# Optimization experiments

Hardware: AMD Instinct MI355X
Metric: run time of the kernel (lower is better)

## Reference

```python
import jax, jax.numpy as jnp
import numpy as np

T = 8           # hardcoded frame count in forward
MAX_D = 3       # hardcoded displacement radius -> 7x7 = 49-entry cost volume
PATCH = 2 * MAX_D + 1
EPS = 1e-12     # F.normalize eps


def _l2norm_c(x):
    # x: [B, C, H, W]; L2-normalize over channel dim (torch F.normalize dim=1)
    n = jnp.sqrt(jnp.sum(x * x, axis=1, keepdims=True))
    return x / jnp.maximum(n, EPS)


def setup_inputs() -> dict:
    key = jax.random.key(0)
    ks = jax.random.split(key, 6)
    B, N, C = 2, 8192, 512
    nh = 8
    d = C // nh
    return {
        "x": jax.random.normal(ks[0], (B, N, C), jnp.float32),
        "w_qk": jax.random.normal(ks[1], (2 * C, C), jnp.float32) * 0.02,
        "w_corr": jax.random.normal(ks[2], (d, PATCH * PATCH), jnp.float32) * 0.02,
        "b_corr": jax.random.normal(ks[3], (d,), jnp.float32) * 0.02,
        "w_proj": jax.random.normal(ks[4], (C, C), jnp.float32) * 0.02,
        "b_proj": jax.random.normal(ks[5], (C,), jnp.float32) * 0.02,
    }


def reference(x, w_qk, w_corr, b_corr, w_proj, b_proj):
    B, N, C = x.shape
    nh = 8
    d = C // nh
    H = int(round((N // T) ** 0.5))
    W = H

    # qk projection (no bias): [B, N, 2C] -> [2, B, nh, N, d]
    qk = jnp.einsum('bnc,ec->bne', x, w_qk).reshape(B, N, 2, nh, d)
    q = jnp.transpose(qk[:, :, 0], (0, 2, 1, 3))  # [B, nh, N, d]
    k = jnp.transpose(qk[:, :, 1], (0, 2, 1, 3))

    # 'b n (t h w) d -> (b n) t d h w'
    def to_vid(a):
        a = a.reshape(B, nh, T, H, W, d)
        return jnp.transpose(a, (0, 1, 2, 5, 3, 4)).reshape(B * nh, T, d, H, W)

    q = to_vid(q)
    k = to_vid(k)

    # k_postfix: shift time forward, repeat last frame
    k_post = jnp.concatenate([k[:, 1:], k[:, -1:]], axis=1)

    BT = B * nh * T
    qf = _l2norm_c(q.reshape(BT, d, H, W))
    kf = _l2norm_c(k_post.reshape(BT, d, H, W))

    # local cost volume: corr[b, u*7+v, y, x] = sum_c qf[b,c,y,x] * kf[b,c,y+u-3,x+v-3]
    kp = jnp.pad(kf, ((0, 0), (0, 0), (MAX_D, MAX_D), (MAX_D, MAX_D)))
    corr = jnp.stack(
        [jnp.sum(qf * kp[:, :, u:u + H, v:v + W], axis=1)
         for u in range(PATCH) for v in range(PATCH)],
        axis=1,
    )  # [BT, 49, H, W]

    # 'b u v h w -> b (h w) (u v)'
    corr = jnp.transpose(corr, (0, 2, 3, 1)).reshape(BT, H * W, PATCH * PATCH)

    # proj_corr: 49 -> head_dim
    mf = jnp.einsum('bpk,dk->bpd', corr, w_corr) + b_corr  # [BT, HW, d]

    # '(b n t) (h w) d -> b (t h w) (n d)'
    mf = mf.reshape(B, nh, T, H, W, d)
    mf = jnp.transpose(mf, (0, 2, 3, 4, 1, 5)).reshape(B, N, C)

    # final projection
    return jnp.einsum('bnc,oc->bno', mf, w_proj) + b_proj
```

## Files before the change

kernel.cpp:

```cpp
#include <hip/hip_runtime.h>

typedef unsigned int u32;
typedef unsigned short u16;
typedef __fp16 h2 __attribute__((ext_vector_type(2)));
typedef __fp16 f16x8 __attribute__((ext_vector_type(8)));
typedef float f32x4 __attribute__((ext_vector_type(4)));

#define DEVFN static __device__ __forceinline__

DEVFN u32 pkh(float a, float b) {
  return __builtin_bit_cast(u32, __builtin_amdgcn_cvt_pkrtz(a, b));
}
DEVFN u16 f2h(float f) { __fp16 h = (__fp16)f; return __builtin_bit_cast(u16, h); }

#if __has_builtin(__builtin_amdgcn_fdot2)
DEVFN float dot2u(u32 a, u32 b, float c) {
  return __builtin_amdgcn_fdot2(__builtin_bit_cast(h2, a),
                                __builtin_bit_cast(h2, b), c, false);
}
#else
DEVFN float dot2u(u32 a, u32 b, float c) {
  h2 x = __builtin_bit_cast(h2, a), y = __builtin_bit_cast(h2, b);
  return c + (float)x[0] * (float)y[0] + (float)x[1] * (float)y[1];
}
#endif

DEVFN uint4 cvt8h(const float* p) {
  f32x4 v0 = *(const f32x4*)p;
  f32x4 v1 = *(const f32x4*)(p + 4);
  uint4 o;
  o.x = pkh(v0.x, v0.y); o.y = pkh(v0.z, v0.w);
  o.z = pkh(v1.x, v1.y); o.w = pkh(v1.z, v1.w);
  return o;
}

DEVFN void gld16(const u16* g, u16* l) {
  __builtin_amdgcn_global_load_lds(
      (const __attribute__((address_space(1))) u32*)g,
      (__attribute__((address_space(3))) u32*)l, 16, 0, 0);
}

__global__ __launch_bounds__(256) void cvt3(
    const float* __restrict__ x, const float* __restrict__ wqk,
    u16* __restrict__ xb, u16* __restrict__ wqb) {
  const size_t e = ((size_t)blockIdx.x * 256 + threadIdx.x) * 8;
  const float* s;
  u16* d;
  if (e < 8388608) { s = x + e; d = xb + e; }
  else { s = wqk + (e - 8388608); d = wqb + (e - 8388608); }
  *(uint4*)d = cvt8h(s);
}

__global__ __launch_bounds__(512) void w2prep(
    const float* __restrict__ wp, const float* __restrict__ wc,
    const float* __restrict__ bc, const float* __restrict__ bp,
    u16* __restrict__ W2, float* __restrict__ cvec) {
  __shared__ float wcl[64 * 49];
  __shared__ float wpl[512];
  const int o = blockIdx.x, tid = threadIdx.x;
  for (int i = tid; i < 64 * 49; i += 512) wcl[i] = wc[i];
  wpl[tid] = wp[o * 512 + tid];
  __syncthreads();
  const int hh = tid >> 6, r = tid & 63, du = r >> 3, dv = r & 7;
  float s = 0.f;
  if (du < 7 && dv < 7) {
#pragma unroll
    for (int c = 0; c < 64; ++c) s += wpl[hh * 64 + c] * wcl[c * 49 + du * 7 + dv];
  }
  W2[o * 512 + tid] = f2h(s);
  if (tid < 64) {
    float p = 0.f;
#pragma unroll
    for (int g = 0; g < 8; ++g) p += wpl[g * 64 + tid];
    p *= bc[tid];
    p += __shfl_xor(p, 1); p += __shfl_xor(p, 2); p += __shfl_xor(p, 4);
    p += __shfl_xor(p, 8); p += __shfl_xor(p, 16); p += __shfl_xor(p, 32);
    if (tid == 0) cvec[o] = p + bp[o];
  }
}

template <int MODE, int TN>
__global__ __launch_bounds__(256) void gemm(
    const u16* __restrict__ A, const u16* __restrict__ B,
    const float* __restrict__ bias, void* __restrict__ Out_,
    int Nn, int K) {
  __shared__ u16 As[128 * 32];
  __shared__ u16 Bs[128 * 32];
  const int tid = threadIdx.x;
  const int lane = tid & 63;
  const int w = tid >> 6;
  const int wm = w >> 1, wn = w & 1;
  const int nwg = (int)gridDim.x;
  const int wg = ((int)blockIdx.x & 7) * (nwg >> 3) + ((int)blockIdx.x >> 3);
  const int tm = wg / TN, tn = wg % TN;

  const int sr = w * 32 + (lane >> 2);
  const int sc = (lane & 3) << 3;
  u16* lA = As + w * 1024;
  u16* lB = Bs + w * 1024;
  const u16* gA = A + (size_t)(tm * 128 + sr) * K + sc;
  const u16* gB = B + (size_t)(tn * 128 + sr) * K + sc;

  const u16* rA = As + (wm * 64 + (lane & 15)) * 32 + ((lane >> 4) << 3);
  const u16* rB = Bs + (wn * 64 + (lane & 15)) * 32 + ((lane >> 4) << 3);

  f32x4 acc[4][4] = {};

  const int KT = K >> 5;
  for (int kt = 0; kt < KT; ++kt) {
    __syncthreads();
    gld16(gA + kt * 32, lA);
    gld16(gA + kt * 32 + (size_t)16 * K, lA + 512);
    gld16(gB + kt * 32, lB);
    gld16(gB + kt * 32 + (size_t)16 * K, lB + 512);
    __syncthreads();
    f16x8 af[4], bf[4];
#pragma unroll
    for (int i = 0; i < 4; ++i) af[i] = *(const f16x8*)(rA + i * 512);
#pragma unroll
    for (int i = 0; i < 4; ++i) bf[i] = *(const f16x8*)(rB + i * 512);
#pragma unroll
    for (int mi = 0; mi < 4; ++mi)
#pragma unroll
      for (int ni = 0; ni < 4; ++ni)
        acc[mi][ni] = __builtin_amdgcn_mfma_f32_16x16x32_f16(af[mi], bf[ni],
                                                             acc[mi][ni], 0, 0, 0);
  }

  const int rowBase = tm * 128 + wm * 64 + ((lane >> 4) << 2);
  const int colBase = tn * 128 + wn * 64 + (lane & 15);

  if (MODE == 1) {
    float* Out = (float*)Out_;
    float bv[4];
#pragma unroll
    for (int ni = 0; ni < 4; ++ni) bv[ni] = bias[colBase + ni * 16];
#pragma unroll
    for (int mi = 0; mi < 4; ++mi)
#pragma unroll
      for (int r = 0; r < 4; ++r) {
        size_t ro = (size_t)(rowBase + mi * 16 + r) * Nn;
#pragma unroll
        for (int ni = 0; ni < 4; ++ni)
          Out[ro + colBase + ni * 16] = acc[mi][ni][r] + bv[ni];
      }
  } else {
    u16* Out = (u16*)Out_;
    const int sel = colBase >> 9;
    const int hh = (colBase >> 6) & 7;
    const int ddb = lane & 15;
#pragma unroll
    for (int mi = 0; mi < 4; ++mi)
#pragma unroll
      for (int r = 0; r < 4; ++r) {
        float s = acc[mi][0][r] * acc[mi][0][r] + acc[mi][1][r] * acc[mi][1][r] +
                  acc[mi][2][r] * acc[mi][2][r] + acc[mi][3][r] * acc[mi][3][r];
        s += __shfl_xor(s, 1);
        s += __shfl_xor(s, 2);
        s += __shfl_xor(s, 4);
        s += __shfl_xor(s, 8);
        float inv = 1.0f / fmaxf(sqrtf(s), 1e-12f);
        const int m = rowBase + mi * 16 + r;
        const int bb = m >> 13, tt = (m >> 10) & 7, pix = m & 1023;
        const int fr = ((sel * 2 + bb) * 8 + tt) * 8 + hh;
        size_t base = (((size_t)fr) << 16) + (size_t)pix * 64 + ddb;
#pragma unroll
        for (int ni = 0; ni < 4; ++ni)
          Out[base + ni * 16] = f2h(acc[mi][ni][r] * inv);
      }
  }
}

__global__ __launch_bounds__(256) void dots(
    const u16* __restrict__ qf, u16* __restrict__ corr) {
  __shared__ __align__(16) u16 kst[448 * 64];
  const int tid = threadIdx.x;
  const int bid = ((int)blockIdx.x & 7) * 64 + ((int)blockIdx.x >> 3);
  const int fr = bid >> 2, grp = bid & 3;
  const int h = fr & 7, t = (fr >> 3) & 7, b = fr >> 6;
  const int t1 = (t < 7) ? t + 1 : 7;
  const int y0 = grp * 8;

  const u16* kbase = qf + (((size_t)(((2 + b) * 8 + t1) * 8 + h)) << 16);
  {
    const int ppx = tid >> 3;
    const int slot = tid & 7;
#pragma unroll
    for (int pass = 0; pass < 14; ++pass) {
      int gy = y0 - 3 + pass;
      uint4 v = make_uint4(0, 0, 0, 0);
      if ((unsigned)gy < 32u)
        v = *(const uint4*)(kbase + (size_t)(gy * 32 + ppx) * 64 + slot * 8);
      int pl = pass * 32 + ppx;
      *(uint4*)((char*)kst + pl * 128 + ((slot * 16) ^ ((pl & 7) << 4))) = v;
    }
  }

  const int px = grp * 256 + tid;
  const int x = tid & 31, yloc = tid >> 5;
  const u16* qp = qf + (((size_t)fr) << 16) + (size_t)px * 64;
  u32 qw[32];
#pragma unroll
  for (int j = 0; j < 8; ++j) {
    uint4 v = *(const uint4*)(qp + j * 8);
    qw[j * 4 + 0] = v.x; qw[j * 4 + 1] = v.y;
    qw[j * 4 + 2] = v.z; qw[j * 4 + 3] = v.w;
  }
  __syncthreads();

  u16* mp = corr + (size_t)((b * 8 + t) * 1024 + px) * 512 + h * 64;
  for (int du = 0; du < 7; ++du) {
    const int rlbase = (yloc + du) * 32;
    float f[7];
#pragma unroll
    for (int dv = 0; dv < 7; ++dv) {
      int xx = x + dv - 3;
      int xc = xx < 0 ? 0 : (xx > 31 ? 31 : xx);
      int pl = rlbase + xc;
      const char* kr = (const char*)kst + pl * 128;
      const int swz = (pl & 7) << 4;
      float s0 = 0.f, s1 = 0.f, s2 = 0.f, s3 = 0.f;
#pragma unroll
      for (int j = 0; j < 8; ++j) {
        uint4 v = *(const uint4*)(kr + ((j * 16) ^ swz));
        s0 = dot2u(qw[j * 4 + 0], v.x, s0);
        s1 = dot2u(qw[j * 4 + 1], v.y, s1);
        s2 = dot2u(qw[j * 4 + 2], v.z, s2);
        s3 = dot2u(qw[j * 4 + 3], v.w, s3);
      }
      float s = (s0 + s1) + (s2 + s3);
      f[dv] = ((unsigned)xx < 32u) ? s : 0.f;
    }
    uint4 o;
    o.x = pkh(f[0], f[1]); o.y = pkh(f[2], f[3]);
    o.z = pkh(f[4], f[5]); o.w = pkh(f[6], 0.f);
    *(uint4*)(mp + du * 8) = o;
  }
  *(uint4*)(mp + 56) = make_uint4(0, 0, 0, 0);
}

extern "C" void kernel_launch(void* const* d_in, const int* in_sizes, int n_in,
                              void* d_out, int out_size, void* d_ws, size_t ws_size,
                              hipStream_t stream) {
  const float* x      = (const float*)d_in[0];
  const float* w_qk   = (const float*)d_in[1];
  const float* w_corr = (const float*)d_in[2];
  const float* b_corr = (const float*)d_in[3];
  const float* w_proj = (const float*)d_in[4];
  const float* b_proj = (const float*)d_in[5];
  float* out = (float*)d_out;

  u16* xb   = (u16*)d_ws;
  u16* corr = xb;
  u16* qf   = (u16*)d_ws + (size_t)16384 * 512;
  u16* W2   = qf;
  float* cvec = (float*)(qf + (size_t)512 * 512);
  u16* wqb  = (u16*)d_out;

  cvt3<<<dim3(4352), dim3(256), 0, stream>>>(x, w_qk, xb, wqb);
  gemm<0, 8><<<dim3(1024), dim3(256), 0, stream>>>(xb, wqb, nullptr, qf,
                                                   1024, 512);
  dots<<<dim3(512), dim3(256), 0, stream>>>(qf, corr);
  w2prep<<<dim3(512), dim3(512), 0, stream>>>(w_proj, w_corr, b_corr, b_proj,
                                              W2, cvec);
  gemm<1, 4><<<dim3(512), dim3(256), 0, stream>>>(corr, W2, cvec, out,
                                                  512, 512);
}
```

Measured before the change: 91.37 us.

## Fuse fp32-to-fp16 conversion into QK GEMM loads and double-buffer LDS

Drops the separate conversion kernel that turned x and w_qk into fp16 in workspace. The QK GEMM now reads fp32 directly from global memory and packs it to fp16 in registers before storing to shared memory. Both GEMMs also gain a double-buffered LDS pipeline that prefetches the next K tile while the MFMAs run on the current one, leaving one barrier per iteration. This removes a kernel launch and a full fp16 write-then-read of the activations, but the QK GEMM reads twice the bytes per tile and uses more registers and shared memory.

```diff
diff --git a/kernel.cpp b/kernel.cpp
--- a/kernel.cpp
+++ b/kernel.cpp
@@ -25,12 +25,10 @@
 }
 #endif
 
-DEVFN uint4 cvt8h(const float* p) {
-  f32x4 v0 = *(const f32x4*)p;
-  f32x4 v1 = *(const f32x4*)(p + 4);
+DEVFN uint4 pk8(f32x4 lo, f32x4 hi) {
   uint4 o;
-  o.x = pkh(v0.x, v0.y); o.y = pkh(v0.z, v0.w);
-  o.z = pkh(v1.x, v1.y); o.w = pkh(v1.z, v1.w);
+  o.x = pkh(lo.x, lo.y); o.y = pkh(lo.z, lo.w);
+  o.z = pkh(hi.x, hi.y); o.w = pkh(hi.z, hi.w);
   return o;
 }
 
@@ -38,17 +36,6 @@
   __builtin_amdgcn_global_load_lds(
       (const __attribute__((address_space(1))) u32*)g,
       (__attribute__((address_space(3))) u32*)l, 16, 0, 0);
-}
-
-__global__ __launch_bounds__(256) void cvt3(
-    const float* __restrict__ x, const float* __restrict__ wqk,
-    u16* __restrict__ xb, u16* __restrict__ wqb) {
-  const size_t e = ((size_t)blockIdx.x * 256 + threadIdx.x) * 8;
-  const float* s;
-  u16* d;
-  if (e < 8388608) { s = x + e; d = xb + e; }
-  else { s = wqk + (e - 8388608); d = wqb + (e - 8388608); }
-  *(uint4*)d = cvt8h(s);
 }
 
 __global__ __launch_bounds__(512) void w2prep(
@@ -79,13 +66,13 @@
   }
 }
 
-template <int MODE, int TN>
+template <int MODE, int AF32, int BF32, int TN>
 __global__ __launch_bounds__(256) void gemm(
-    const u16* __restrict__ A, const u16* __restrict__ B,
+    const void* __restrict__ A_, const void* __restrict__ B_,
     const float* __restrict__ bias, void* __restrict__ Out_,
     int Nn, int K) {
-  __shared__ u16 As[128 * 32];
-  __shared__ u16 Bs[128 * 32];
+  __shared__ u16 As[2][128 * 32];
+  __shared__ u16 Bs[2][128 * 32];
   const int tid = threadIdx.x;
   const int lane = tid & 63;
   const int w = tid >> 6;
@@ -94,37 +81,103 @@
   const int wg = ((int)blockIdx.x & 7) * (nwg >> 3) + ((int)blockIdx.x >> 3);
   const int tm = wg / TN, tn = wg % TN;
 
+  const float* Af = (const float*)A_;
+  const float* Bf = (const float*)B_;
+  const u16* Ah = (const u16*)A_;
+  const u16* Bh = (const u16*)B_;
+
   const int sr = w * 32 + (lane >> 2);
   const int sc = (lane & 3) << 3;
-  u16* lA = As + w * 1024;
-  u16* lB = Bs + w * 1024;
-  const u16* gA = A + (size_t)(tm * 128 + sr) * K + sc;
-  const u16* gB = B + (size_t)(tn * 128 + sr) * K + sc;
-
-  const u16* rA = As + (wm * 64 + (lane & 15)) * 32 + ((lane >> 4) << 3);
-  const u16* rB = Bs + (wn * 64 + (lane & 15)) * 32 + ((lane >> 4) << 3);
+  const u16* gA = Ah + (size_t)(tm * 128 + sr) * K + sc;
+  const u16* gB = Bh + (size_t)(tn * 128 + sr) * K + sc;
+  u16* lA = &As[0][0] + w * 1024;
+  u16* lB = &Bs[0][0] + w * 1024;
+
+  const int rr = tid >> 2;
+  const int rc = (tid & 3) << 3;
+  const size_t offA0 = (size_t)(tm * 128 + rr) * K + rc;
+  const size_t offB0 = (size_t)(tn * 128 + rr) * K + rc;
+  u16* sA0 = &As[0][0] + rr * 32 + rc;
+  u16* sB0 = &Bs[0][0] + rr * 32 + rc;
+
+  const u16* rA = &As[0][0] + (wm * 64 + (lane & 15)) * 32 + ((lane >> 4) << 3);
+  const u16* rB = &Bs[0][0] + (wn * 64 + (lane & 15)) * 32 + ((lane >> 4) << 3);
 
   f32x4 acc[4][4] = {};
-
   const int KT = K >> 5;
+
+  if (AF32) {
+    f32x4 p0 = *(const f32x4*)(Af + offA0);
+    f32x4 p1 = *(const f32x4*)(Af + offA0 + 4);
+    f32x4 p2 = *(const f32x4*)(Af + offA0 + (size_t)64 * K);
+    f32x4 p3 = *(const f32x4*)(Af + offA0 + (size_t)64 * K + 4);
+    *(uint4*)sA0 = pk8(p0, p1);
+    *(uint4*)(sA0 + 2048) = pk8(p2, p3);
+  } else {
+    gld16(gA, lA);
+    gld16(gA + (size_t)16 * K, lA + 512);
+  }
+  if (BF32) {
+    f32x4 p0 = *(const f32x4*)(Bf + offB0);
+    f32x4 p1 = *(const f32x4*)(Bf + offB0 + 4);
+    f32x4 p2 = *(const f32x4*)(Bf + offB0 + (size_t)64 * K);
+    f32x4 p3 = *(const f32x4*)(Bf + offB0 + (size_t)64 * K + 4);
+    *(uint4*)sB0 = pk8(p0, p1);
+    *(uint4*)(sB0 + 2048) = pk8(p2, p3);
+  } else {
+    gld16(gB, lB);
+    gld16(gB + (size_t)16 * K, lB + 512);
+  }
+  __syncthreads();
+
   for (int kt = 0; kt < KT; ++kt) {
-    __syncthreads();
-    gld16(gA + kt * 32, lA);
-    gld16(gA + kt * 32 + (size_t)16 * K, lA + 512);
-    gld16(gB + kt * 32, lB);
-    gld16(gB + kt * 32 + (size_t)16 * K, lB + 512);
-    __syncthreads();
+    const int cur = kt & 1, nxt = cur ^ 1;
+    const bool more = (kt + 1) < KT;
+    f32x4 a0, a1, a2, a3, b0, b1, b2, b3;
+    if (more) {
+      const int off = (kt + 1) * 32;
+      if (AF32) {
+        a0 = *(const f32x4*)(Af + offA0 + off);
+        a1 = *(const f32x4*)(Af + offA0 + off + 4);
+        a2 = *(const f32x4*)(Af + offA0 + off + (size_t)64 * K);
+        a3 = *(const f32x4*)(Af + offA0 + off + (size_t)64 * K + 4);
+      } else {
+        gld16(gA + off, lA + nxt * 4096);
+        gld16(gA + off + (size_t)16 * K, lA + nxt * 4096 + 512);
+      }
+      if (BF32) {
+        b0 = *(const f32x4*)(Bf + offB0 + off);
+        b1 = *(const f32x4*)(Bf + offB0 + off + 4);
+        b2 = *(const f32x4*)(Bf + offB0 + off + (size_t)64 * K);
+        b3 = *(const f32x4*)(Bf + offB0 + off + (size_t)64 * K + 4);
+      } else {
+        gld16(gB + off, lB + nxt * 4096);
+        gld16(gB + off + (size_t)16 * K, lB + nxt * 4096 + 512);
+      }
+    }
+
     f16x8 af[4], bf[4];
 #pragma unroll
-    for (int i = 0; i < 4; ++i) af[i] = *(const f16x8*)(rA + i * 512);
-#pragma unroll
-    for (int i = 0; i < 4; ++i) bf[i] = *(const f16x8*)(rB + i * 512);
+    for (int i = 0; i < 4; ++i) af[i] = *(const f16x8*)(rA + cur * 4096 + i * 512);
+#pragma unroll
+    for (int i = 0; i < 4; ++i) bf[i] = *(const f16x8*)(rB + cur * 4096 + i * 512);
 #pragma unroll
     for (int mi = 0; mi < 4; ++mi)
 #pragma unroll
       for (int ni = 0; ni < 4; ++ni)
         acc[mi][ni] = __builtin_amdgcn_mfma_f32_16x16x32_f16(af[mi], bf[ni],
                                                              acc[mi][ni], 0, 0, 0);
+    if (more) {
+      if (AF32) {
+        *(uint4*)(sA0 + nxt * 4096) = pk8(a0, a1);
+        *(uint4*)(sA0 + nxt * 4096 + 2048) = pk8(a2, a3);
+      }
+      if (BF32) {
+        *(uint4*)(sB0 + nxt * 4096) = pk8(b0, b1);
+        *(uint4*)(sB0 + nxt * 4096 + 2048) = pk8(b2, b3);
+      }
+    }
+    __syncthreads();
   }
 
   const int rowBase = tm * 128 + wm * 64 + ((lane >> 4) << 2);
@@ -250,19 +303,16 @@
   const float* b_proj = (const float*)d_in[5];
   float* out = (float*)d_out;
 
-  u16* xb   = (u16*)d_ws;
-  u16* corr = xb;
-  u16* qf   = (u16*)d_ws + (size_t)16384 * 512;
+  u16* corr = (u16*)d_ws;
+  u16* qf   = corr + (size_t)16384 * 512;
   u16* W2   = qf;
   float* cvec = (float*)(qf + (size_t)512 * 512);
-  u16* wqb  = (u16*)d_out;
-
-  cvt3<<<dim3(4352), dim3(256), 0, stream>>>(x, w_qk, xb, wqb);
-  gemm<0, 8><<<dim3(1024), dim3(256), 0, stream>>>(xb, wqb, nullptr, qf,
-                                                   1024, 512);
+
+  gemm<0, 1, 1, 8><<<dim3(1024), dim3(256), 0, stream>>>(
+      x, w_qk, nullptr, qf, 1024, 512);
   dots<<<dim3(512), dim3(256), 0, stream>>>(qf, corr);
   w2prep<<<dim3(512), dim3(512), 0, stream>>>(w_proj, w_corr, b_corr, b_proj,
                                               W2, cvec);
-  gemm<1, 4><<<dim3(512), dim3(256), 0, stream>>>(corr, W2, cvec, out,
-                                                  512, 512);
-}
+  gemm<1, 0, 0, 4><<<dim3(512), dim3(256), 0, stream>>>(
+      corr, W2, cvec, out, 512, 512);
+}
```

After: 83.73 us. 8.4% less time.

## Fuse fp32->fp16 conversion into GEMM loads, double-buffer LDS, merge weight prep

Applied to the files above, without the earlier changes.

Removes the standalone conversion kernel. The first GEMM now reads fp32 x and w_qk directly and packs them to fp16 into LDS, which avoids writing and re-reading the fp16 copies. The GEMM switches from global_load_lds to register-staged loads with double-buffered LDS, prefetching two tiles ahead so loads overlap MFMA work. The weight-combination prep is folded into the cost-volume kernel as extra blocks, cutting one launch. The trade-offs are more register pressure and twice the fp32 global traffic per tile in the first GEMM.

```diff
diff --git a/kernel.cpp b/kernel.cpp
--- a/kernel.cpp
+++ b/kernel.cpp
@@ -25,67 +25,20 @@
 }
 #endif
 
-DEVFN uint4 cvt8h(const float* p) {
-  f32x4 v0 = *(const f32x4*)p;
-  f32x4 v1 = *(const f32x4*)(p + 4);
+DEVFN uint4 pk8(f32x4 lo, f32x4 hi) {
   uint4 o;
-  o.x = pkh(v0.x, v0.y); o.y = pkh(v0.z, v0.w);
-  o.z = pkh(v1.x, v1.y); o.w = pkh(v1.z, v1.w);
+  o.x = pkh(lo.x, lo.y); o.y = pkh(lo.z, lo.w);
+  o.z = pkh(hi.x, hi.y); o.w = pkh(hi.z, hi.w);
   return o;
 }
 
-DEVFN void gld16(const u16* g, u16* l) {
-  __builtin_amdgcn_global_load_lds(
-      (const __attribute__((address_space(1))) u32*)g,
-      (__attribute__((address_space(3))) u32*)l, 16, 0, 0);
-}
-
-__global__ __launch_bounds__(256) void cvt3(
-    const float* __restrict__ x, const float* __restrict__ wqk,
-    u16* __restrict__ xb, u16* __restrict__ wqb) {
-  const size_t e = ((size_t)blockIdx.x * 256 + threadIdx.x) * 8;
-  const float* s;
-  u16* d;
-  if (e < 8388608) { s = x + e; d = xb + e; }
-  else { s = wqk + (e - 8388608); d = wqb + (e - 8388608); }
-  *(uint4*)d = cvt8h(s);
-}
-
-__global__ __launch_bounds__(512) void w2prep(
-    const float* __restrict__ wp, const float* __restrict__ wc,
-    const float* __restrict__ bc, const float* __restrict__ bp,
-    u16* __restrict__ W2, float* __restrict__ cvec) {
-  __shared__ float wcl[64 * 49];
-  __shared__ float wpl[512];
-  const int o = blockIdx.x, tid = threadIdx.x;
-  for (int i = tid; i < 64 * 49; i += 512) wcl[i] = wc[i];
-  wpl[tid] = wp[o * 512 + tid];
-  __syncthreads();
-  const int hh = tid >> 6, r = tid & 63, du = r >> 3, dv = r & 7;
-  float s = 0.f;
-  if (du < 7 && dv < 7) {
-#pragma unroll
-    for (int c = 0; c < 64; ++c) s += wpl[hh * 64 + c] * wcl[c * 49 + du * 7 + dv];
-  }
-  W2[o * 512 + tid] = f2h(s);
-  if (tid < 64) {
-    float p = 0.f;
-#pragma unroll
-    for (int g = 0; g < 8; ++g) p += wpl[g * 64 + tid];
-    p *= bc[tid];
-    p += __shfl_xor(p, 1); p += __shfl_xor(p, 2); p += __shfl_xor(p, 4);
-    p += __shfl_xor(p, 8); p += __shfl_xor(p, 16); p += __shfl_xor(p, 32);
-    if (tid == 0) cvec[o] = p + bp[o];
-  }
-}
-
-template <int MODE, int TN>
+template <int MODE, int F32, int TN>
 __global__ __launch_bounds__(256) void gemm(
-    const u16* __restrict__ A, const u16* __restrict__ B,
+    const void* __restrict__ A_, const void* __restrict__ B_,
     const float* __restrict__ bias, void* __restrict__ Out_,
     int Nn, int K) {
-  __shared__ u16 As[128 * 32];
-  __shared__ u16 Bs[128 * 32];
+  __shared__ u16 As[2][4096];
+  __shared__ u16 Bs[2][4096];
   const int tid = threadIdx.x;
   const int lane = tid & 63;
   const int w = tid >> 6;
@@ -94,38 +47,90 @@
   const int wg = ((int)blockIdx.x & 7) * (nwg >> 3) + ((int)blockIdx.x >> 3);
   const int tm = wg / TN, tn = wg % TN;
 
-  const int sr = w * 32 + (lane >> 2);
-  const int sc = (lane & 3) << 3;
-  u16* lA = As + w * 1024;
-  u16* lB = Bs + w * 1024;
-  const u16* gA = A + (size_t)(tm * 128 + sr) * K + sc;
-  const u16* gB = B + (size_t)(tn * 128 + sr) * K + sc;
-
-  const u16* rA = As + (wm * 64 + (lane & 15)) * 32 + ((lane >> 4) << 3);
-  const u16* rB = Bs + (wn * 64 + (lane & 15)) * 32 + ((lane >> 4) << 3);
+  const float* Af = (const float*)A_;
+  const float* Bf = (const float*)B_;
+  const u16* Ah = (const u16*)A_;
+  const u16* Bh = (const u16*)B_;
+
+  const int rr = tid >> 2;
+  const int s8 = (tid & 3) << 3;
+  const size_t offA = (size_t)(tm * 128 + rr) * K + s8;
+  const size_t offB = (size_t)(tn * 128 + rr) * K + s8;
+  const int wofs = rr * 32 + s8;
+
+  const int rofsA = ((wm * 64 + (lane & 15)) << 5) + ((lane >> 4) << 3);
+  const int rofsB = ((wn * 64 + (lane & 15)) << 5) + ((lane >> 4) << 3);
 
   f32x4 acc[4][4] = {};
-
   const int KT = K >> 5;
+
+  f32x4 a0, a1, a2, a3, b0, b1, b2, b3;
+  uint4 ha0, ha1, hb0, hb1;
+
+#define ISSUE(t)                                                          \
+  {                                                                       \
+    const size_t oa = offA + (size_t)(t) * 32;                            \
+    const size_t ob = offB + (size_t)(t) * 32;                            \
+    if (F32) {                                                            \
+      a0 = *(const f32x4*)(Af + oa);                                      \
+      a1 = *(const f32x4*)(Af + oa + 4);                                  \
+      a2 = *(const f32x4*)(Af + oa + (size_t)64 * K);                     \
+      a3 = *(const f32x4*)(Af + oa + (size_t)64 * K + 4);                 \
+      b0 = *(const f32x4*)(Bf + ob);                                      \
+      b1 = *(const f32x4*)(Bf + ob + 4);                                  \
+      b2 = *(const f32x4*)(Bf + ob + (size_t)64 * K);                     \
+      b3 = *(const f32x4*)(Bf + ob + (size_t)64 * K + 4);                 \
+    } else {                                                              \
+      ha0 = *(const uint4*)(Ah + oa);                                     \
+      ha1 = *(const uint4*)(Ah + oa + (size_t)64 * K);                    \
+      hb0 = *(const uint4*)(Bh + ob);                                     \
+      hb1 = *(const uint4*)(Bh + ob + (size_t)64 * K);                    \
+    }                                                                     \
+  }
+
+#define WRITE(bufi)                                                       \
+  {                                                                       \
+    u16* da = &As[bufi][wofs];                                            \
+    u16* db = &Bs[bufi][wofs];                                            \
+    if (F32) {                                                            \
+      *(uint4*)da = pk8(a0, a1);                                          \
+      *(uint4*)(da + 2048) = pk8(a2, a3);                                 \
+      *(uint4*)db = pk8(b0, b1);                                          \
+      *(uint4*)(db + 2048) = pk8(b2, b3);                                 \
+    } else {                                                              \
+      *(uint4*)da = ha0;                                                  \
+      *(uint4*)(da + 2048) = ha1;                                         \
+      *(uint4*)db = hb0;                                                  \
+      *(uint4*)(db + 2048) = hb1;                                         \
+    }                                                                     \
+  }
+
+  ISSUE(0)
+  WRITE(0)
+  ISSUE(1)
+  __syncthreads();
+
   for (int kt = 0; kt < KT; ++kt) {
-    __syncthreads();
-    gld16(gA + kt * 32, lA);
-    gld16(gA + kt * 32 + (size_t)16 * K, lA + 512);
-    gld16(gB + kt * 32, lB);
-    gld16(gB + kt * 32 + (size_t)16 * K, lB + 512);
-    __syncthreads();
+    const int cur = kt & 1;
+    if (kt + 1 < KT) {
+      WRITE(cur ^ 1)
+      if (kt + 2 < KT) ISSUE(kt + 2)
+    }
     f16x8 af[4], bf[4];
 #pragma unroll
-    for (int i = 0; i < 4; ++i) af[i] = *(const f16x8*)(rA + i * 512);
-#pragma unroll
-    for (int i = 0; i < 4; ++i) bf[i] = *(const f16x8*)(rB + i * 512);
+    for (int i = 0; i < 4; ++i) af[i] = *(const f16x8*)(&As[cur][rofsA + i * 512]);
+#pragma unroll
+    for (int i = 0; i < 4; ++i) bf[i] = *(const f16x8*)(&Bs[cur][rofsB + i * 512]);
 #pragma unroll
     for (int mi = 0; mi < 4; ++mi)
 #pragma unroll
       for (int ni = 0; ni < 4; ++ni)
         acc[mi][ni] = __builtin_amdgcn_mfma_f32_16x16x32_f16(af[mi], bf[ni],
                                                              acc[mi][ni], 0, 0, 0);
-  }
+    __syncthreads();
+  }
+#undef ISSUE
+#undef WRITE
 
   const int rowBase = tm * 128 + wm * 64 + ((lane >> 4) << 2);
   const int colBase = tn * 128 + wn * 64 + (lane & 15);
@@ -171,10 +176,47 @@
   }
 }
 
-__global__ __launch_bounds__(256) void dots(
-    const u16* __restrict__ qf, u16* __restrict__ corr) {
-  __shared__ __align__(16) u16 kst[448 * 64];
+__global__ __launch_bounds__(256) void dots_w2(
+    const u16* __restrict__ qf, u16* __restrict__ corr,
+    const float* __restrict__ wp, const float* __restrict__ wc,
+    const float* __restrict__ bc, const float* __restrict__ bp,
+    u16* __restrict__ W2, float* __restrict__ cvec) {
+  __shared__ __align__(16) u16 smem[448 * 64];
   const int tid = threadIdx.x;
+
+  if ((int)blockIdx.x >= 512) {
+    const int o = (int)blockIdx.x - 512;
+    float* wcl = (float*)smem;
+    float* wpl = wcl + 3136;
+    for (int i = tid; i < 3136; i += 256) wcl[i] = wc[i];
+    wpl[tid] = wp[o * 512 + tid];
+    wpl[tid + 256] = wp[o * 512 + tid + 256];
+    __syncthreads();
+#pragma unroll
+    for (int pass = 0; pass < 2; ++pass) {
+      const int idx = pass * 256 + tid;
+      const int hh = idx >> 6, r = idx & 63, du = r >> 3, dv = r & 7;
+      float sv = 0.f;
+      if (du < 7 && dv < 7) {
+#pragma unroll
+        for (int c = 0; c < 64; ++c)
+          sv += wpl[hh * 64 + c] * wcl[c * 49 + du * 7 + dv];
+      }
+      W2[o * 512 + idx] = f2h(sv);
+    }
+    if (tid < 64) {
+      float p = 0.f;
+#pragma unroll
+      for (int g = 0; g < 8; ++g) p += wpl[g * 64 + tid];
+      p *= bc[tid];
+      p += __shfl_xor(p, 1); p += __shfl_xor(p, 2); p += __shfl_xor(p, 4);
+      p += __shfl_xor(p, 8); p += __shfl_xor(p, 16); p += __shfl_xor(p, 32);
+      if (tid == 0) cvec[o] = p + bp[o];
+    }
+    return;
+  }
+
+  u16* kst = smem;
   const int bid = ((int)blockIdx.x & 7) * 64 + ((int)blockIdx.x >> 3);
   const int fr = bid >> 2, grp = bid & 3;
   const int h = fr & 7, t = (fr >> 3) & 7, b = fr >> 6;
@@ -250,19 +292,15 @@
   const float* b_proj = (const float*)d_in[5];
   float* out = (float*)d_out;
 
-  u16* xb   = (u16*)d_ws;
-  u16* corr = xb;
-  u16* qf   = (u16*)d_ws + (size_t)16384 * 512;
-  u16* W2   = qf;
-  float* cvec = (float*)(qf + (size_t)512 * 512);
-  u16* wqb  = (u16*)d_out;
-
-  cvt3<<<dim3(4352), dim3(256), 0, stream>>>(x, w_qk, xb, wqb);
-  gemm<0, 8><<<dim3(1024), dim3(256), 0, stream>>>(xb, wqb, nullptr, qf,
-                                                   1024, 512);
-  dots<<<dim3(512), dim3(256), 0, stream>>>(qf, corr);
-  w2prep<<<dim3(512), dim3(512), 0, stream>>>(w_proj, w_corr, b_corr, b_proj,
-                                              W2, cvec);
-  gemm<1, 4><<<dim3(512), dim3(256), 0, stream>>>(corr, W2, cvec, out,
-                                                  512, 512);
-}
+  u16* corr = (u16*)d_ws;
+  u16* qf   = corr + (size_t)16384 * 512;
+  u16* W2   = qf + (size_t)16384 * 1024;
+  float* cvec = (float*)(W2 + (size_t)512 * 512);
+
+  gemm<0, 1, 8><<<dim3(1024), dim3(256), 0, stream>>>(
+      x, w_qk, nullptr, qf, 1024, 512);
+  dots_w2<<<dim3(1024), dim3(256), 0, stream>>>(qf, corr, w_proj, w_corr,
+                                                b_corr, b_proj, W2, cvec);
+  gemm<1, 0, 4><<<dim3(512), dim3(256), 0, stream>>>(
+      corr, W2, cvec, out, 512, 512);
+}
```

Measured after the change: 79.47 us. 1.15x faster.
